# Kernel optimization log

Measured on AMD Instinct MI355X. Metric: run time of the kernel, lower is better.

## Reference

```python
import jax, jax.numpy as jnp
import numpy as np

NUM_HEADS = 16

def setup_inputs() -> dict:
    key = jax.random.key(0)
    k1, k2, k3 = jax.random.split(key, 3)
    B, N, C = 2, 2048, 1024
    x = jax.random.normal(k1, (B, N, C), dtype=jnp.float32)
    # Dense layers: qkv (C -> 3C, no bias), proj (C -> C, with bias)
    w_qkv = jax.random.normal(k2, (C, 3 * C), dtype=jnp.float32) * (C ** -0.5)
    w_proj = jax.random.normal(k3, (C, C), dtype=jnp.float32) * (C ** -0.5)
    b_proj = jnp.zeros((C,), dtype=jnp.float32)
    return {"x": x, "w_qkv": w_qkv, "w_proj": w_proj, "b_proj": b_proj}

def reference(x, w_qkv, w_proj, b_proj):
    B, N, C = x.shape
    H = NUM_HEADS
    Dh = C // H
    scale = Dh ** -0.5
    qkv = x @ w_qkv                                   # [B,N,3C]
    qkv = qkv.reshape(B, N, 3, H, Dh)
    qkv = jnp.transpose(qkv, (2, 0, 3, 1, 4))         # [3,B,H,N,Dh]
    q, k, v = qkv[0], qkv[1], qkv[2]
    attn = jnp.einsum('bhnd,bhmd->bhnm', q, k) * scale  # [B,H,N,N]
    attn = jax.nn.softmax(attn, axis=-1)
    out = jnp.einsum('bhnm,bhmd->bhnd', attn, v)        # [B,H,N,Dh]
    out = jnp.transpose(out, (0, 2, 1, 3)).reshape(B, N, C)
    return out @ w_proj + b_proj
```

## Files before the change

### kernel.cpp

```cpp
#include <hip/hip_runtime.h>
#include <stdint.h>


typedef unsigned short u16;
typedef uint32_t u32;
typedef __bf16 bf16x8 __attribute__((ext_vector_type(8)));
typedef unsigned short u16x8 __attribute__((ext_vector_type(8)));
typedef float f32x4 __attribute__((ext_vector_type(4)));
typedef float f32x16 __attribute__((ext_vector_type(16)));
typedef uint32_t u32x4v __attribute__((ext_vector_type(4)));

#define DEV static __device__ __forceinline__

DEV u16 f2bf(float f) {
    uint32_t u = __float_as_uint(f);
    u += 0x7fffu + ((u >> 16) & 1u);
    return (u16)(u >> 16);
}

DEV u32 cvtpk(float lo, float hi_) {
    u32 r;
    asm("v_cvt_pk_bf16_f32 %0, %1, %2" : "=v"(r) : "v"(lo), "v"(hi_));
    return r;
}
DEV void plswap(u32& x, u32& y) {
    asm("v_permlane32_swap_b32 %0, %1" : "+v"(x), "+v"(y));
}
DEV float exp2f_fast(float x) {
    float r;
    asm("v_exp_f32 %0, %1" : "=v"(r) : "v"(x));
    return r;
}

DEV void gload_lds16(const void* g, void* l) {
    __builtin_amdgcn_global_load_lds(
        (const __attribute__((address_space(1))) uint32_t*)g,
        (__attribute__((address_space(3))) uint32_t*)l, 16, 0, 0);
}

#define WAIT_VM(N) asm volatile("s_waitcnt vmcnt(" #N ")" ::: "memory")
#define RAW_BAR() __builtin_amdgcn_s_barrier()
#define SCHED_PIN() __builtin_amdgcn_sched_barrier(0)

DEV bf16x8 swz_load16(const u16* base, int row, int kbyte) {
    int off = (row * 128 + kbyte) ^ ((row & 7) << 4);
    return *reinterpret_cast<const bf16x8*>(reinterpret_cast<const char*>(base) + off);
}

__global__ __launch_bounds__(256) void prep_kernel(
    const float* __restrict__ x, u16* __restrict__ xb,
    const float* __restrict__ wq, u16* __restrict__ wqt,
    const float* __restrict__ wp, u16* __restrict__ wpt) {
    __shared__ float T[32][33];
    int b = blockIdx.x, tid = threadIdx.x;
    if (b < 2048) {
        int t = b * 256 + tid;
        const float4* p = reinterpret_cast<const float4*>(x) + (size_t)t * 2;
        float4 a = p[0], c = p[1];
        u16x8 o;
        o[0] = f2bf(a.x); o[1] = f2bf(a.y); o[2] = f2bf(a.z); o[3] = f2bf(a.w);
        o[4] = f2bf(c.x); o[5] = f2bf(c.y); o[6] = f2bf(c.z); o[7] = f2bf(c.w);
        reinterpret_cast<u16x8*>(xb)[t] = o;
        return;
    }
    const float* in;
    u16* out;
    int bx, by, R = 1024, Cc;
    if (b < 5120) {
        int idx = b - 2048;
        bx = idx % 96; by = idx / 96; Cc = 3072; in = wq; out = wqt;
    } else {
        int idx = b - 5120;
        bx = idx % 32; by = idx / 32; Cc = 1024; in = wp; out = wpt;
    }
    int tx = tid & 31, ty = tid >> 5;
    int xcol = bx * 32 + tx;
    int y0 = by * 32;
#pragma unroll
    for (int i = 0; i < 4; i++) {
        int y = y0 + ty + i * 8;
        T[ty + i * 8][tx] = in[(size_t)y * Cc + xcol];
    }
    __syncthreads();
    int xo = y0 + tx;
    int yo0 = bx * 32;
#pragma unroll
    for (int i = 0; i < 4; i++) {
        int yo = yo0 + ty + i * 8;
        out[(size_t)yo * R + xo] = f2bf(T[tx][ty + i * 8]);
    }
}

__global__ void trv_kernel(const u16* __restrict__ v, u16* __restrict__ vt) {
    __shared__ u16 T[64][72];
    int bh = blockIdx.y, t = blockIdx.x, tid = threadIdx.x;
    const u16* vb = v + (size_t)bh * 2048 * 64;
    u16* vo = vt + (size_t)bh * 64 * 2048;
#pragma unroll
    for (int i = 0; i < 2; i++) {
        int c = tid + i * 256, row = c >> 3, c8 = c & 7;
        u16x8 a = *reinterpret_cast<const u16x8*>(vb + (size_t)(t * 64 + row) * 64 + c8 * 8);
#pragma unroll
        for (int j = 0; j < 8; j++) T[row][c8 * 8 + j] = a[j];
    }
    __syncthreads();
#pragma unroll
    for (int i = 0; i < 2; i++) {
        int c = tid + i * 256, drow = c >> 3, c8 = c & 7;
        u16x8 o;
#pragma unroll
        for (int j = 0; j < 8; j++) o[j] = T[c8 * 8 + j][drow];
        *reinterpret_cast<u16x8*>(vo + (size_t)drow * 2048 + t * 64 + c8 * 8) = o;
    }
}


template <int EPI>
__global__ __launch_bounds__(256, 2) void gemm_kernel(
    const u16* __restrict__ A, const u16* __restrict__ Bt, int ntiles,
    u16* __restrict__ o_q, u16* __restrict__ o_k, u16* __restrict__ o_v,
    float* __restrict__ o_f, const float* __restrict__ bias) {
    __shared__ __align__(16) u16 Al[8192];
    __shared__ __align__(16) u16 Bl[8192];
    int tid = threadIdx.x;
    int p = blockIdx.x;
    int xcd = p & 7, q = p >> 3;
    int bm = xcd * 4 + q / ntiles, bn = q % ntiles;
    int lane = tid & 63, w = tid >> 6;
    int wr = w >> 1, wc = w & 1;
    int l15 = lane & 15, lhi = lane >> 4;

    f32x4 acc[4][4];
#pragma unroll
    for (int i = 0; i < 4; i++)
#pragma unroll
        for (int j = 0; j < 4; j++) acc[i][j] = (f32x4){0.f, 0.f, 0.f, 0.f};

    for (int kt = 0; kt < 16; ++kt) {
#pragma unroll
        for (int i = 0; i < 4; i++) {
            int lin = w * 4096 + i * 1024 + lane * 16;
            int row = lin >> 7;
            int src = (lin & 127) ^ ((row & 7) << 4);
            gload_lds16((const char*)A + (size_t)(bm * 128 + row) * 2048 + (size_t)kt * 128 + src,
                        (char*)Al + lin);
            gload_lds16((const char*)Bt + (size_t)(bn * 128 + row) * 2048 + (size_t)kt * 128 + src,
                        (char*)Bl + lin);
        }
        __syncthreads();
#pragma unroll
        for (int ks = 0; ks < 2; ++ks) {
            bf16x8 af[4], bfr[4];
#pragma unroll
            for (int mi = 0; mi < 4; ++mi) af[mi] = swz_load16(Al, wr * 64 + mi * 16 + l15, ks * 64 + lhi * 16);
#pragma unroll
            for (int ni = 0; ni < 4; ++ni) bfr[ni] = swz_load16(Bl, wc * 64 + ni * 16 + l15, ks * 64 + lhi * 16);
            __builtin_amdgcn_s_setprio(1);
#pragma unroll
            for (int mi = 0; mi < 4; ++mi)
#pragma unroll
                for (int ni = 0; ni < 4; ++ni)
                    acc[mi][ni] = __builtin_amdgcn_mfma_f32_16x16x32_bf16(af[mi], bfr[ni], acc[mi][ni], 0, 0, 0);
            __builtin_amdgcn_s_setprio(0);
        }
        __syncthreads();
    }

    int row0 = bm * 128 + wr * 64, col0 = bn * 128 + wc * 64;
    if (EPI == 0) {
#pragma unroll
        for (int mi = 0; mi < 4; mi++)
#pragma unroll
            for (int ni = 0; ni < 4; ni++) {
                int col = col0 + ni * 16 + l15;
                int sel = col >> 10, cc = col & 1023;
                int h = cc >> 6, d = cc & 63;
#pragma unroll
                for (int j = 0; j < 4; j++) {
                    int r = row0 + mi * 16 + lhi * 4 + j;
                    int b = r >> 11, n = r & 2047;
                    size_t idx = (((size_t)(b * 16 + h)) * 2048 + n) * 64 + d;
                    float v = acc[mi][ni][j];
                    if (sel == 0) o_q[idx] = f2bf(v * 0.18033688f);
                    else if (sel == 1) o_k[idx] = f2bf(v);
                    else o_v[idx] = f2bf(v);
                }
            }
    } else {
#pragma unroll
        for (int mi = 0; mi < 4; mi++)
#pragma unroll
            for (int ni = 0; ni < 4; ni++) {
                int col = col0 + ni * 16 + l15;
                float bb = bias[col];
#pragma unroll
                for (int j = 0; j < 4; j++) {
                    int r = row0 + mi * 16 + lhi * 4 + j;
                    o_f[(size_t)r * 1024 + col] = acc[mi][ni][j] + bb;
                }
            }
    }
}

__global__ __launch_bounds__(512, 4) void flash6_kernel(
    const u16* __restrict__ qg, const u16* __restrict__ kg, const u16* __restrict__ vtg,
    u16* __restrict__ o) {
    __shared__ __align__(16) char smem[65536];

    int tid = threadIdx.x, lane = tid & 63, w = tid >> 6;
    int wg = w & 3, g = w >> 2;
    int l31 = lane & 31, hi = lane >> 5;
    int p = blockIdx.y * 16 + blockIdx.x;
    int bh = p & 31, qt = p >> 5;
    int q0 = qt * 128 + wg * 32;

#define KL(gg, bb) (smem + ((gg) * 2 + (bb)) * 8192)
#define VL(gg, bb) (smem + 32768 + ((gg) * 2 + (bb)) * 8192)

    const u16* qp = qg + ((size_t)bh * 2048 + q0 + l31) * 64 + hi * 8;
    bf16x8 qf[4];
#pragma unroll
    for (int ds = 0; ds < 4; ds++) qf[ds] = *reinterpret_cast<const bf16x8*>(qp + ds * 16);

    const char* kbg = (const char*)(kg + (size_t)bh * 2048 * 64) + (size_t)g * 16 * 8192;
    const char* vbg = (const char*)(vtg + (size_t)bh * 64 * 2048) + (size_t)g * 2048;

    int srow = lane >> 1, sinner = (lane & 1) * 16;
    int fbase = l31 * 32 + hi * 16;

#define STAGE(bb, tt)                                                                     \
    {                                                                                     \
        _Pragma("unroll") for (int i = 0; i < 2; i++) {                                   \
            gload_lds16(kbg + (size_t)(tt) * 8192 + (i * 32 + srow) * 128 + wg * 32 + sinner, \
                        KL(g, bb) + wg * 2048 + i * 1024 + lane * 16);                    \
            gload_lds16(vbg + (size_t)(i * 32 + srow) * 4096 + (size_t)(tt) * 128 + wg * 32 + sinner, \
                        VL(g, bb) + wg * 2048 + i * 1024 + lane * 16);                    \
        }                                                                                 \
    }

    f32x16 accO[2];
#pragma unroll
    for (int db = 0; db < 2; db++)
#pragma unroll
        for (int r = 0; r < 16; r++) accO[db][r] = 0.f;
    float lsum = 0.f;

    STAGE(0, 0);

    for (int pp = 0; pp < 16; ++pp) {
        int c = pp & 1;
        if (pp < 15) {
            STAGE(c ^ 1, pp + 1);
            WAIT_VM(4);
        } else {
            WAIT_VM(0);
        }
        RAW_BAR();
        SCHED_PIN();

        bf16x8 ka[2][4];
#pragma unroll
        for (int kvb = 0; kvb < 2; kvb++)
#pragma unroll
            for (int ds = 0; ds < 4; ds++)
                ka[kvb][ds] = *reinterpret_cast<const bf16x8*>(KL(g, c) + ds * 2048 + kvb * 1024 + fbase);
        f32x16 s[2];
        __builtin_amdgcn_s_setprio(1);
#pragma unroll
        for (int kvb = 0; kvb < 2; kvb++) {
#pragma unroll
            for (int r = 0; r < 16; r++) s[kvb][r] = 0.f;
#pragma unroll
            for (int ds = 0; ds < 4; ds++)
                s[kvb] = __builtin_amdgcn_mfma_f32_32x32x16_bf16(ka[kvb][ds], qf[ds], s[kvb], 0, 0, 0);
        }
        __builtin_amdgcn_s_setprio(0);

#pragma unroll
        for (int kvb = 0; kvb < 2; kvb++)
#pragma unroll
            for (int r = 0; r < 16; r++) s[kvb][r] = exp2f_fast(s[kvb][r]);
        float t_[8];
#pragma unroll
        for (int r = 0; r < 8; r++)
            t_[r] = (s[0][r] + s[0][r + 8]) + (s[1][r] + s[1][r + 8]);
#pragma unroll
        for (int r = 0; r < 4; r++) t_[r] += t_[r + 4];
        lsum += (t_[0] + t_[1]) + (t_[2] + t_[3]);

        bf16x8 pb[4];
#pragma unroll
        for (int kvb = 0; kvb < 2; kvb++) {
            u32 x0 = cvtpk(s[kvb][0], s[kvb][1]), y0 = cvtpk(s[kvb][4], s[kvb][5]);
            u32 x1 = cvtpk(s[kvb][2], s[kvb][3]), y1 = cvtpk(s[kvb][6], s[kvb][7]);
            u32 x2 = cvtpk(s[kvb][8], s[kvb][9]), y2 = cvtpk(s[kvb][12], s[kvb][13]);
            u32 x3 = cvtpk(s[kvb][10], s[kvb][11]), y3 = cvtpk(s[kvb][14], s[kvb][15]);
            plswap(x0, y0); plswap(x1, y1); plswap(x2, y2); plswap(x3, y3);
            u32x4v plo = {x0, x1, y0, y1};
            u32x4v phi = {x2, x3, y2, y3};
            pb[2 * kvb] = __builtin_bit_cast(bf16x8, plo);
            pb[2 * kvb + 1] = __builtin_bit_cast(bf16x8, phi);
        }

        bf16x8 va[2][4];
#pragma unroll
        for (int db = 0; db < 2; db++)
#pragma unroll
            for (int ks = 0; ks < 4; ks++)
                va[db][ks] = *reinterpret_cast<const bf16x8*>(VL(g, c) + ks * 2048 + db * 1024 + fbase);
        __builtin_amdgcn_s_setprio(1);
#pragma unroll
        for (int db = 0; db < 2; db++)
#pragma unroll
            for (int ks = 0; ks < 4; ks++)
                accO[db] = __builtin_amdgcn_mfma_f32_32x32x16_bf16(va[db][ks], pb[ks], accO[db], 0, 0, 0);
        __builtin_amdgcn_s_setprio(0);

        RAW_BAR();
    }
#undef STAGE

    lsum += __shfl_xor(lsum, 32);

    float* mbuf = (float*)smem;
    int base = (wg * 64 + lane) * 36;
    if (g == 1) {
#pragma unroll
        for (int db = 0; db < 2; db++)
#pragma unroll
            for (int q4 = 0; q4 < 4; q4++) {
                f32x4 v4 = {accO[db][q4 * 4 + 0], accO[db][q4 * 4 + 1],
                            accO[db][q4 * 4 + 2], accO[db][q4 * 4 + 3]};
                *reinterpret_cast<f32x4*>(mbuf + base + db * 16 + q4 * 4) = v4;
            }
        mbuf[base + 32] = lsum;
    }
    __syncthreads();
    if (g == 0) {
        float lsum2 = mbuf[base + 32];
        float inv = 1.f / (lsum + lsum2);
        int b = bh >> 4, h = bh & 15;
        u16* ob = o + ((size_t)(b * 2048 + q0 + l31)) * 1024 + h * 64;
#pragma unroll
        for (int db = 0; db < 2; db++) {
            f32x4 m4[4];
#pragma unroll
            for (int q4 = 0; q4 < 4; q4++)
                m4[q4] = *reinterpret_cast<const f32x4*>(mbuf + base + db * 16 + q4 * 4);
#pragma unroll
            for (int i = 0; i < 8; i++) {
                int r = 2 * i;
                int d = (r & 3) + 8 * (r >> 2) + 4 * hi + 32 * db;
                float lo = (accO[db][r] + m4[r >> 2][r & 3]) * inv;
                float hi_ = (accO[db][r + 1] + m4[(r + 1) >> 2][(r + 1) & 3]) * inv;
                *reinterpret_cast<u32*>(ob + d) = cvtpk(lo, hi_);
            }
        }
    }
#undef KL
#undef VL
}


extern "C" void kernel_launch(void* const* d_in, const int* in_sizes, int n_in,
                              void* d_out, int out_size, void* d_ws, size_t ws_size,
                              hipStream_t stream) {
    (void)in_sizes; (void)n_in; (void)out_size; (void)ws_size;
    const float* x = (const float*)d_in[0];
    const float* w_qkv = (const float*)d_in[1];
    const float* w_proj = (const float*)d_in[2];
    const float* b_proj = (const float*)d_in[3];
    float* out = (float*)d_out;
    char* ws = (char*)d_ws;

    u16* xb   = (u16*)(ws + 0);
    u16* wqt  = (u16*)(ws + 8388608);
    u16* wpt  = (u16*)(ws + 14680064);
    u16* qws  = (u16*)(ws + 16777216);
    u16* kws  = (u16*)(ws + 25165824);
    u16* vws  = (u16*)(ws + 33554432);
    u16* vtws = (u16*)(ws + 41943040);
    u16* attn = (u16*)(ws + 50331648);

    prep_kernel<<<6144, 256, 0, stream>>>(x, xb, w_qkv, wqt, w_proj, wpt);
    gemm_kernel<0><<<32 * 24, 256, 0, stream>>>(xb, wqt, 24, qws, kws, vws, nullptr, nullptr);
    trv_kernel<<<dim3(32, 32), 256, 0, stream>>>(vws, vtws);
    flash6_kernel<<<dim3(16, 32), 512, 0, stream>>>(qws, kws, vtws, attn);
    gemm_kernel<1><<<32 * 8, 256, 0, stream>>>(attn, wpt, 8, nullptr, nullptr, nullptr, out, b_proj);
}
```

Baseline: 107.7 us.

## Fuse V transpose into QKV GEMM epilogue and compute softmax row sums via MFMA

```diff
diff --git a/kernel.cpp b/kernel.cpp
--- a/kernel.cpp
+++ b/kernel.cpp
@@ -8,6 +8,7 @@
 typedef unsigned short u16x8 __attribute__((ext_vector_type(8)));
 typedef float f32x4 __attribute__((ext_vector_type(4)));
 typedef float f32x16 __attribute__((ext_vector_type(16)));
+typedef uint32_t u32x2v __attribute__((ext_vector_type(2)));
 typedef uint32_t u32x4v __attribute__((ext_vector_type(4)));
 
 #define DEV static __device__ __forceinline__
@@ -91,34 +92,11 @@
     }
 }
 
-__global__ void trv_kernel(const u16* __restrict__ v, u16* __restrict__ vt) {
-    __shared__ u16 T[64][72];
-    int bh = blockIdx.y, t = blockIdx.x, tid = threadIdx.x;
-    const u16* vb = v + (size_t)bh * 2048 * 64;
-    u16* vo = vt + (size_t)bh * 64 * 2048;
-#pragma unroll
-    for (int i = 0; i < 2; i++) {
-        int c = tid + i * 256, row = c >> 3, c8 = c & 7;
-        u16x8 a = *reinterpret_cast<const u16x8*>(vb + (size_t)(t * 64 + row) * 64 + c8 * 8);
-#pragma unroll
-        for (int j = 0; j < 8; j++) T[row][c8 * 8 + j] = a[j];
-    }
-    __syncthreads();
-#pragma unroll
-    for (int i = 0; i < 2; i++) {
-        int c = tid + i * 256, drow = c >> 3, c8 = c & 7;
-        u16x8 o;
-#pragma unroll
-        for (int j = 0; j < 8; j++) o[j] = T[c8 * 8 + j][drow];
-        *reinterpret_cast<u16x8*>(vo + (size_t)drow * 2048 + t * 64 + c8 * 8) = o;
-    }
-}
-
 
 template <int EPI>
 __global__ __launch_bounds__(256, 2) void gemm_kernel(
     const u16* __restrict__ A, const u16* __restrict__ Bt, int ntiles,
-    u16* __restrict__ o_q, u16* __restrict__ o_k, u16* __restrict__ o_v,
+    u16* __restrict__ o_q, u16* __restrict__ o_k, u16* __restrict__ o_vt,
     float* __restrict__ o_f, const float* __restrict__ bias) {
     __shared__ __align__(16) u16 Al[8192];
     __shared__ __align__(16) u16 Bl[8192];
@@ -175,15 +153,20 @@
                 int col = col0 + ni * 16 + l15;
                 int sel = col >> 10, cc = col & 1023;
                 int h = cc >> 6, d = cc & 63;
-#pragma unroll
-                for (int j = 0; j < 4; j++) {
-                    int r = row0 + mi * 16 + lhi * 4 + j;
-                    int b = r >> 11, n = r & 2047;
-                    size_t idx = (((size_t)(b * 16 + h)) * 2048 + n) * 64 + d;
-                    float v = acc[mi][ni][j];
-                    if (sel == 0) o_q[idx] = f2bf(v * 0.18033688f);
-                    else if (sel == 1) o_k[idx] = f2bf(v);
-                    else o_v[idx] = f2bf(v);
+                int r0 = row0 + mi * 16 + lhi * 4;
+                int b = r0 >> 11, n0 = r0 & 2047;
+                if (sel == 2) {
+                    u32x2v pk2 = {cvtpk(acc[mi][ni][0], acc[mi][ni][1]),
+                                  cvtpk(acc[mi][ni][2], acc[mi][ni][3])};
+                    *reinterpret_cast<u32x2v*>(o_vt + ((size_t)(b * 16 + h) * 64 + d) * 2048 + n0) = pk2;
+                } else {
+                    size_t base = (((size_t)(b * 16 + h)) * 2048 + n0) * 64 + d;
+#pragma unroll
+                    for (int j = 0; j < 4; j++) {
+                        float v = acc[mi][ni][j];
+                        if (sel == 0) o_q[base + (size_t)j * 64] = f2bf(v * 0.18033688f);
+                        else o_k[base + (size_t)j * 64] = f2bf(v);
+                    }
                 }
             }
     } else {
@@ -238,12 +221,17 @@
         }                                                                                 \
     }
 
-    f32x16 accO[2];
-#pragma unroll
-    for (int db = 0; db < 2; db++)
-#pragma unroll
-        for (int r = 0; r < 16; r++) accO[db][r] = 0.f;
-    float lsum = 0.f;
+    f32x16 fzero;
+#pragma unroll
+    for (int r = 0; r < 16; r++) fzero[r] = 0.f;
+    f32x16 accO[2], accL;
+#pragma unroll
+    for (int db = 0; db < 2; db++) accO[db] = fzero;
+    accL = fzero;
+    u16x8 ou;
+#pragma unroll
+    for (int j = 0; j < 8; j++) ou[j] = 0x3F80;
+    bf16x8 ones = __builtin_bit_cast(bf16x8, ou);
 
     STAGE(0, 0);
 
@@ -268,10 +256,9 @@
         __builtin_amdgcn_s_setprio(1);
 #pragma unroll
         for (int kvb = 0; kvb < 2; kvb++) {
-#pragma unroll
-            for (int r = 0; r < 16; r++) s[kvb][r] = 0.f;
-#pragma unroll
-            for (int ds = 0; ds < 4; ds++)
+            s[kvb] = __builtin_amdgcn_mfma_f32_32x32x16_bf16(ka[kvb][0], qf[0], fzero, 0, 0, 0);
+#pragma unroll
+            for (int ds = 1; ds < 4; ds++)
                 s[kvb] = __builtin_amdgcn_mfma_f32_32x32x16_bf16(ka[kvb][ds], qf[ds], s[kvb], 0, 0, 0);
         }
         __builtin_amdgcn_s_setprio(0);
@@ -280,13 +267,6 @@
         for (int kvb = 0; kvb < 2; kvb++)
 #pragma unroll
             for (int r = 0; r < 16; r++) s[kvb][r] = exp2f_fast(s[kvb][r]);
-        float t_[8];
-#pragma unroll
-        for (int r = 0; r < 8; r++)
-            t_[r] = (s[0][r] + s[0][r + 8]) + (s[1][r] + s[1][r + 8]);
-#pragma unroll
-        for (int r = 0; r < 4; r++) t_[r] += t_[r + 4];
-        lsum += (t_[0] + t_[1]) + (t_[2] + t_[3]);
 
         bf16x8 pb[4];
 #pragma unroll
@@ -310,17 +290,18 @@
                 va[db][ks] = *reinterpret_cast<const bf16x8*>(VL(g, c) + ks * 2048 + db * 1024 + fbase);
         __builtin_amdgcn_s_setprio(1);
 #pragma unroll
-        for (int db = 0; db < 2; db++)
-#pragma unroll
-            for (int ks = 0; ks < 4; ks++)
-                accO[db] = __builtin_amdgcn_mfma_f32_32x32x16_bf16(va[db][ks], pb[ks], accO[db], 0, 0, 0);
+        for (int ks = 0; ks < 4; ks++) {
+            accO[0] = __builtin_amdgcn_mfma_f32_32x32x16_bf16(va[0][ks], pb[ks], accO[0], 0, 0, 0);
+            accO[1] = __builtin_amdgcn_mfma_f32_32x32x16_bf16(va[1][ks], pb[ks], accO[1], 0, 0, 0);
+            accL = __builtin_amdgcn_mfma_f32_32x32x16_bf16(ones, pb[ks], accL, 0, 0, 0);
+        }
         __builtin_amdgcn_s_setprio(0);
 
         RAW_BAR();
     }
 #undef STAGE
 
-    lsum += __shfl_xor(lsum, 32);
+    float lsum = accL[0];
 
     float* mbuf = (float*)smem;
     int base = (wg * 64 + lane) * 36;
@@ -378,13 +359,11 @@
     u16* wpt  = (u16*)(ws + 14680064);
     u16* qws  = (u16*)(ws + 16777216);
     u16* kws  = (u16*)(ws + 25165824);
-    u16* vws  = (u16*)(ws + 33554432);
     u16* vtws = (u16*)(ws + 41943040);
     u16* attn = (u16*)(ws + 50331648);
 
     prep_kernel<<<6144, 256, 0, stream>>>(x, xb, w_qkv, wqt, w_proj, wpt);
-    gemm_kernel<0><<<32 * 24, 256, 0, stream>>>(xb, wqt, 24, qws, kws, vws, nullptr, nullptr);
-    trv_kernel<<<dim3(32, 32), 256, 0, stream>>>(vws, vtws);
+    gemm_kernel<0><<<32 * 24, 256, 0, stream>>>(xb, wqt, 24, qws, kws, vtws, nullptr, nullptr);
     flash6_kernel<<<dim3(16, 32), 512, 0, stream>>>(qws, kws, vtws, attn);
     gemm_kernel<1><<<32 * 8, 256, 0, stream>>>(attn, wpt, 8, nullptr, nullptr, nullptr, out, b_proj);
 }
```

Result: faster. 103.3 us (-4.1%).
